# Kernel optimization log

Hardware: AMD Instinct MI355X
Metric: run time of the kernel (lower is better)

Reference implementation:

```python
import jax, jax.numpy as jnp
import numpy as np

EMBED_DIM = 768
FFN_DIM = 3072
N_WIRES = 10


def setup_inputs() -> dict:
    key = jax.random.key(0)
    ks = jax.random.split(key, 7)
    x = jax.random.normal(ks[0], (8, 2048, EMBED_DIM), dtype=jnp.float32)
    # map_to_wires: nn.Linear(embed_dim, n_wires, bias=False) -> weight [n_wires, embed_dim]
    W_map = jax.random.normal(ks[1], (N_WIRES, EMBED_DIM), dtype=jnp.float32) / np.sqrt(EMBED_DIM)
    # trainable RY rotation angles, one per wire
    theta = jax.random.uniform(ks[2], (N_WIRES,), dtype=jnp.float32, minval=-np.pi, maxval=np.pi)
    W1 = jax.random.normal(ks[3], (FFN_DIM, N_WIRES), dtype=jnp.float32) / np.sqrt(N_WIRES)
    b1 = jnp.zeros((FFN_DIM,), dtype=jnp.float32)
    W2 = jax.random.normal(ks[4], (EMBED_DIM, FFN_DIM), dtype=jnp.float32) / np.sqrt(FFN_DIM)
    b2 = jnp.zeros((EMBED_DIM,), dtype=jnp.float32)
    return {"x": x, "W_map": W_map, "theta": theta, "W1": W1, "b1": b1, "W2": W2, "b2": b2}


def reference(x, W_map, theta, W1, b1, W2, b2):
    batch, seq_len, embed_dim = x.shape
    x_flat = x.reshape(batch * seq_len, embed_dim)            # [F, E]
    x_wires = x_flat @ W_map.T                                 # [F, W]
    # Quantum circuit: per wire i, state RY(theta_i) RX(x_i) |0>.
    # All gates are single-qubit on the |0...0> product state, so the
    # register stays a product state and <Z_i> reduces exactly to
    # cos(theta_i) * cos(x_i) (same math as the full 2^n statevector sim).
    q_out = jnp.cos(theta)[None, :] * jnp.cos(x_wires)         # [F, W]
    h = jax.nn.relu(q_out @ W1.T + b1)                         # [F, FFN]
    out = h @ W2.T + b2                                        # [F, E]
    return out.reshape(batch, seq_len, embed_dim)
```

## Files before the change

### kernel.cpp

```cpp
#include <hip/hip_runtime.h>
#include <hip/hip_bf16.h>


typedef __attribute__((ext_vector_type(4))) float f32x4;
typedef __attribute__((ext_vector_type(8))) short bf16x8;

#define F_TOTAL 16384
#define E_DIM   768
#define FFN     3072

static __device__ __forceinline__ unsigned short f2bf(float f) {
    union { float f; unsigned int i; } v; v.f = f;
    unsigned int r = v.i + 0x7FFFu + ((v.i >> 16) & 1u);
    return (unsigned short)(r >> 16);
}
static __device__ __forceinline__ unsigned int pkbf(float a, float b) {
    __hip_bfloat162 h2 = __float22bfloat162_rn(float2{a, b});
    union { __hip_bfloat162 h; unsigned int u; } v; v.h = h2; return v.u;
}
static __device__ __forceinline__ void gload16(const void* g, void* l) {
    __builtin_amdgcn_global_load_lds((const __attribute__((address_space(1))) unsigned int*)g,
                                     (__attribute__((address_space(3))) unsigned int*)l,
                                     16, 0, 0);
}

__global__ __launch_bounds__(384) void kW2(const float* __restrict__ w2,
                                           unsigned short* __restrict__ w2b) {
    const int n = (int)blockIdx.x;
    const int c = (int)threadIdx.x;
    const float4* src = (const float4*)(w2 + (size_t)n * FFN + c * 8);
    float4 a = src[0], b = src[1];
    bf16x8 v;
    v[0] = (short)f2bf(a.x); v[1] = (short)f2bf(a.y);
    v[2] = (short)f2bf(a.z); v[3] = (short)f2bf(a.w);
    v[4] = (short)f2bf(b.x); v[5] = (short)f2bf(b.y);
    v[6] = (short)f2bf(b.z); v[7] = (short)f2bf(b.w);
    *(bf16x8*)(w2b + (size_t)n * FFN + (size_t)(c ^ (n & 7)) * 8) = v;
}

__global__ void kP(const float* __restrict__ w1,
                   const float* __restrict__ b1,
                   unsigned short* __restrict__ w1p) {
    int k = blockIdx.x * 256 + threadIdx.x;
    if (k >= FFN) return;
    float r[32];
#pragma unroll
    for (int w = 0; w < 10; ++w) r[w] = w1[k * 10 + w];
    r[10] = b1[k];
#pragma unroll
    for (int w = 11; w < 32; ++w) r[w] = 0.f;
#pragma unroll
    for (int c = 0; c < 4; ++c) {
        bf16x8 v;
#pragma unroll
        for (int e = 0; e < 8; ++e) v[e] = (short)f2bf(r[c * 8 + e]);
        *(bf16x8*)(w1p + (size_t)k * 32 + (size_t)((c ^ (k & 3)) * 8)) = v;
    }
}

__global__ __launch_bounds__(256) void kQ(const float* __restrict__ x,
                                          const float* __restrict__ wm,
                                          const float* __restrict__ th,
                                          unsigned short* __restrict__ qp) {
    __shared__ float wms[10 * 768];
    const int tid = (int)threadIdx.x;
    for (int i = tid; i < 10 * 768; i += 256) wms[i] = wm[i];
    __syncthreads();

    const int wv = tid >> 6, l = tid & 63;
    const int mbase = (int)blockIdx.x * 16 + wv * 4;
    const float thv = (l < 10) ? th[l] : 0.f;
    const float cth = __cosf(thv);

#pragma unroll
    for (int r = 0; r < 4; ++r) {
        const int m = mbase + r;
        const float4* xp = (const float4*)(x + (size_t)m * E_DIM);
        const float4 xa = xp[l], xb = xp[64 + l], xc = xp[128 + l];
        float s[10];
#pragma unroll
        for (int w = 0; w < 10; ++w) {
            const float4* wp = (const float4*)(wms + w * E_DIM);
            const float4 wa = wp[l], wb = wp[64 + l], wc = wp[128 + l];
            float t0 = xa.x * wa.x;
            float t1 = xa.y * wa.y;
            t0 = fmaf(xa.z, wa.z, t0); t1 = fmaf(xa.w, wa.w, t1);
            t0 = fmaf(xb.x, wb.x, t0); t1 = fmaf(xb.y, wb.y, t1);
            t0 = fmaf(xb.z, wb.z, t0); t1 = fmaf(xb.w, wb.w, t1);
            t0 = fmaf(xc.x, wc.x, t0); t1 = fmaf(xc.y, wc.y, t1);
            t0 = fmaf(xc.z, wc.z, t0); t1 = fmaf(xc.w, wc.w, t1);
            s[w] = t0 + t1;
        }
#pragma unroll
        for (int w = 0; w < 10; ++w) {
            float v = s[w];
            v += __shfl_xor(v, 1);  v += __shfl_xor(v, 2);  v += __shfl_xor(v, 4);
            v += __shfl_xor(v, 8);  v += __shfl_xor(v, 16); v += __shfl_xor(v, 32);
            s[w] = v;
        }
        if (l < 32) {
            float sv = 0.f;
#pragma unroll
            for (int w = 0; w < 10; ++w) sv = (l == w) ? s[w] : sv;
            float val = (l < 10) ? (cth * __cosf(sv)) : ((l == 10) ? 1.0f : 0.f);
            qp[(size_t)m * 32 + (size_t)((((l >> 3) ^ (m & 3)) * 8) + (l & 7))] = f2bf(val);
        }
    }
}

__global__ __launch_bounds__(512, 4) void kG(const unsigned short* __restrict__ w2b,
                                             const float* __restrict__ b2,
                                             const unsigned short* __restrict__ qp,
                                             const unsigned short* __restrict__ w1p,
                                             float* __restrict__ outp) {
    __shared__ __align__(16) unsigned short w2s[2][192 * 64];
    __shared__ __align__(16) unsigned short hs[128 * 64];

    const int tid = (int)threadIdx.x;
    const int wv = tid >> 6, l = tid & 63;
    const int bid = (int)blockIdx.x;
    const int x8 = bid & 7, yb = bid >> 3;
    const int m0 = ((x8 & 1) * 64 + yb) * 128;
    const int n0 = (x8 >> 1) * 192;

    const int rw = tid >> 3, cw = tid & 7;
    const int wr = wv >> 2, wc = wv & 3;

    int hwo[4];
    {
        const int hm = wv * 16 + (l & 15);
        const int kb = (l >> 4) * 4;
#pragma unroll
        for (int ki = 0; ki < 4; ++ki) {
            int k = ki * 16 + kb;
            int c = k >> 3;
            hwo[ki] = hm * 64 + ((c ^ (hm & 7)) * 8) + (k & 7);
        }
    }

#define STAGE(BUF, KT) do { int k0_ = (KT) * 64;                                   \
    _Pragma("unroll") for (int i_ = 0; i_ < 3; ++i_) {                             \
        int r_ = i_ * 64 + rw;                                                     \
        gload16(w2b + (size_t)(n0 + r_) * FFN + k0_ + (size_t)cw * 8,              \
                (unsigned short*)w2s[BUF] + i_ * 4096 + wv * 512); } } while (0)

#define LOADW1(D, KT, KI) do {                                                     \
    const unsigned short* a_ = w1p + (size_t)((KT) * 64 + (KI) * 16 + (l & 15)) * 32 \
                                   + (size_t)(((l >> 4) ^ (l & 3)) * 8);           \
    asm volatile("global_load_dwordx4 %0, %1, off" : "=v"(D) : "v"(a_)); } while (0)

    bf16x8 aq;
    {
        const unsigned short* qa = qp + (size_t)(m0 + wv * 16 + (l & 15)) * 32
                                      + (size_t)(((l >> 4) ^ (l & 3)) * 8);
        asm volatile("global_load_dwordx4 %0, %1, off" : "=v"(aq) : "v"(qa));
    }
    bf16x8 f0, f1, f2, f3, g0, g1, g2, g3;
    STAGE(0, 0);
    LOADW1(f0, 0, 0); LOADW1(f1, 0, 1); LOADW1(f2, 0, 2); LOADW1(f3, 0, 3);

    const f32x4 z4 = {0.f, 0.f, 0.f, 0.f};
    f32x4 acc[4][3];
#pragma unroll
    for (int a = 0; a < 4; ++a)
#pragma unroll
        for (int b = 0; b < 3; ++b) acc[a][b] = z4;

    int cur = 0;
    for (int t = 0; t < 48; ++t) {
        asm volatile("s_waitcnt vmcnt(0)" ::: "memory");
        __builtin_amdgcn_sched_barrier(0);
        __builtin_amdgcn_s_barrier();
        __builtin_amdgcn_sched_barrier(0);

        if (t < 47) {
            STAGE(cur ^ 1, t + 1);
            LOADW1(g0, t + 1, 0); LOADW1(g1, t + 1, 1);
            LOADW1(g2, t + 1, 2); LOADW1(g3, t + 1, 3);
        }

        {
            f32x4 hv0 = __builtin_amdgcn_mfma_f32_16x16x32_bf16(f0, aq, z4, 0, 0, 0);
            f32x4 hv1 = __builtin_amdgcn_mfma_f32_16x16x32_bf16(f1, aq, z4, 0, 0, 0);
            f32x4 hv2 = __builtin_amdgcn_mfma_f32_16x16x32_bf16(f2, aq, z4, 0, 0, 0);
            f32x4 hv3 = __builtin_amdgcn_mfma_f32_16x16x32_bf16(f3, aq, z4, 0, 0, 0);
            uint2 pw;
            pw.x = pkbf(fmaxf(hv0[0], 0.f), fmaxf(hv0[1], 0.f));
            pw.y = pkbf(fmaxf(hv0[2], 0.f), fmaxf(hv0[3], 0.f));
            *(uint2*)(hs + hwo[0]) = pw;
            pw.x = pkbf(fmaxf(hv1[0], 0.f), fmaxf(hv1[1], 0.f));
            pw.y = pkbf(fmaxf(hv1[2], 0.f), fmaxf(hv1[3], 0.f));
            *(uint2*)(hs + hwo[1]) = pw;
            pw.x = pkbf(fmaxf(hv2[0], 0.f), fmaxf(hv2[1], 0.f));
            pw.y = pkbf(fmaxf(hv2[2], 0.f), fmaxf(hv2[3], 0.f));
            *(uint2*)(hs + hwo[2]) = pw;
            pw.x = pkbf(fmaxf(hv3[0], 0.f), fmaxf(hv3[1], 0.f));
            pw.y = pkbf(fmaxf(hv3[2], 0.f), fmaxf(hv3[3], 0.f));
            *(uint2*)(hs + hwo[3]) = pw;
        }

        asm volatile("s_waitcnt lgkmcnt(0)" ::: "memory");
        __builtin_amdgcn_sched_barrier(0);
        __builtin_amdgcn_s_barrier();
        __builtin_amdgcn_sched_barrier(0);

        {
            const unsigned short* w2c = (const unsigned short*)w2s[cur];
#pragma unroll
            for (int kk2 = 0; kk2 < 2; ++kk2) {
                const int kc = kk2 * 4 + (l >> 4);
                bf16x8 af[4], bfr[3];
#pragma unroll
                for (int mi = 0; mi < 4; ++mi) {
                    int m_ = wr * 64 + mi * 16 + (l & 15);
                    af[mi] = *(const bf16x8*)(hs + m_ * 64 + ((kc ^ (m_ & 7)) * 8));
                }
#pragma unroll
                for (int ni = 0; ni < 3; ++ni) {
                    int n_ = wc * 48 + ni * 16 + (l & 15);
                    bfr[ni] = *(const bf16x8*)(w2c + n_ * 64 + ((kc ^ (n_ & 7)) * 8));
                }
                __builtin_amdgcn_s_setprio(1);
#pragma unroll
                for (int ni = 0; ni < 3; ++ni)
#pragma unroll
                    for (int mi = 0; mi < 4; ++mi)
                        acc[mi][ni] = __builtin_amdgcn_mfma_f32_16x16x32_bf16(af[mi], bfr[ni], acc[mi][ni], 0, 0, 0);
                __builtin_amdgcn_s_setprio(0);
            }
        }

        f0 = g0; f1 = g1; f2 = g2; f3 = g3;
        cur ^= 1;
    }
#undef STAGE
#undef LOADW1

#pragma unroll
    for (int ni = 0; ni < 3; ++ni) {
        int n = n0 + wc * 48 + ni * 16 + (l & 15);
        float b2v = b2[n];
#pragma unroll
        for (int mi = 0; mi < 4; ++mi) {
            int mb = m0 + wr * 64 + mi * 16 + (l >> 4) * 4;
#pragma unroll
            for (int jj = 0; jj < 4; ++jj)
                outp[(size_t)(mb + jj) * E_DIM + n] = acc[mi][ni][jj] + b2v;
        }
    }
}

extern "C" void kernel_launch(void* const* d_in, const int* in_sizes, int n_in,
                              void* d_out, int out_size, void* d_ws, size_t ws_size,
                              hipStream_t stream) {
    const float* x    = (const float*)d_in[0];
    const float* wmap = (const float*)d_in[1];
    const float* th   = (const float*)d_in[2];
    const float* w1   = (const float*)d_in[3];
    const float* b1   = (const float*)d_in[4];
    const float* w2   = (const float*)d_in[5];
    const float* b2   = (const float*)d_in[6];
    float* out = (float*)d_out;

    unsigned short* qp  = (unsigned short*)d_ws;
    unsigned short* w1p = qp + (size_t)F_TOTAL * 32;
    unsigned short* w2b = w1p + (size_t)FFN * 32;

    kW2<<<E_DIM, 384, 0, stream>>>(w2, w2b);
    kP<<<(FFN + 255) / 256, 256, 0, stream>>>(w1, b1, w1p);
    kQ<<<1024, 256, 0, stream>>>(x, wmap, th, qp);
    kG<<<512, 512, 0, stream>>>(w2b, b2, qp, w1p, out);
}
```

Before: 124.2 us.

## Load W2 fragments directly from global into registers instead of LDS staging

Drops the double-buffered LDS staging of W2 tiles via global_load_lds. Each wave now reads its W2 B-fragments straight from global memory into registers every iteration, and the W2 swizzle in the conversion kernel is removed to match. The W1 prefetch switches from inline asm to plain loads issued after the first GEMM. This frees LDS and a sync wait, but relies on L2/L1 to cover the W2 reads that the four row-waves repeat, and it loses explicit latency hiding since the loads are used in the same iteration.

```diff
diff --git a/kernel.cpp b/kernel.cpp
--- a/kernel.cpp
+++ b/kernel.cpp
@@ -17,11 +17,6 @@
 static __device__ __forceinline__ unsigned int pkbf(float a, float b) {
     __hip_bfloat162 h2 = __float22bfloat162_rn(float2{a, b});
     union { __hip_bfloat162 h; unsigned int u; } v; v.h = h2; return v.u;
-}
-static __device__ __forceinline__ void gload16(const void* g, void* l) {
-    __builtin_amdgcn_global_load_lds((const __attribute__((address_space(1))) unsigned int*)g,
-                                     (__attribute__((address_space(3))) unsigned int*)l,
-                                     16, 0, 0);
 }
 
 __global__ __launch_bounds__(384) void kW2(const float* __restrict__ w2,
@@ -35,7 +30,7 @@
     v[2] = (short)f2bf(a.z); v[3] = (short)f2bf(a.w);
     v[4] = (short)f2bf(b.x); v[5] = (short)f2bf(b.y);
     v[6] = (short)f2bf(b.z); v[7] = (short)f2bf(b.w);
-    *(bf16x8*)(w2b + (size_t)n * FFN + (size_t)(c ^ (n & 7)) * 8) = v;
+    *(bf16x8*)(w2b + (size_t)n * FFN + (size_t)c * 8) = v;
 }
 
 __global__ void kP(const float* __restrict__ w1,
@@ -113,7 +108,6 @@
                                              const unsigned short* __restrict__ qp,
                                              const unsigned short* __restrict__ w1p,
                                              float* __restrict__ outp) {
-    __shared__ __align__(16) unsigned short w2s[2][192 * 64];
     __shared__ __align__(16) unsigned short hs[128 * 64];
 
     const int tid = (int)threadIdx.x;
@@ -123,7 +117,6 @@
     const int m0 = ((x8 & 1) * 64 + yb) * 128;
     const int n0 = (x8 >> 1) * 192;
 
-    const int rw = tid >> 3, cw = tid & 7;
     const int wr = wv >> 2, wc = wv & 3;
 
     int hwo[4];
@@ -138,26 +131,18 @@
         }
     }
 
-#define STAGE(BUF, KT) do { int k0_ = (KT) * 64;                                   \
-    _Pragma("unroll") for (int i_ = 0; i_ < 3; ++i_) {                             \
-        int r_ = i_ * 64 + rw;                                                     \
-        gload16(w2b + (size_t)(n0 + r_) * FFN + k0_ + (size_t)cw * 8,              \
-                (unsigned short*)w2s[BUF] + i_ * 4096 + wv * 512); } } while (0)
-
-#define LOADW1(D, KT, KI) do {                                                     \
-    const unsigned short* a_ = w1p + (size_t)((KT) * 64 + (KI) * 16 + (l & 15)) * 32 \
-                                   + (size_t)(((l >> 4) ^ (l & 3)) * 8);           \
-    asm volatile("global_load_dwordx4 %0, %1, off" : "=v"(D) : "v"(a_)); } while (0)
-
-    bf16x8 aq;
-    {
-        const unsigned short* qa = qp + (size_t)(m0 + wv * 16 + (l & 15)) * 32
-                                      + (size_t)(((l >> 4) ^ (l & 3)) * 8);
-        asm volatile("global_load_dwordx4 %0, %1, off" : "=v"(aq) : "v"(qa));
-    }
-    bf16x8 f0, f1, f2, f3, g0, g1, g2, g3;
-    STAGE(0, 0);
-    LOADW1(f0, 0, 0); LOADW1(f1, 0, 1); LOADW1(f2, 0, 2); LOADW1(f3, 0, 3);
+    const unsigned short* p2[3];
+#pragma unroll
+    for (int ni = 0; ni < 3; ++ni)
+        p2[ni] = w2b + (size_t)(n0 + wc * 48 + ni * 16 + (l & 15)) * FFN + (l >> 4) * 8;
+    const unsigned short* p1 = w1p + (l & 15) * 32 + ((l >> 4) ^ (l & 3)) * 8;
+
+    bf16x8 aq = *(const bf16x8*)(qp + (size_t)(m0 + wv * 16 + (l & 15)) * 32
+                                    + (size_t)(((l >> 4) ^ (l & 3)) * 8));
+    bf16x8 f0 = *(const bf16x8*)(p1);
+    bf16x8 f1 = *(const bf16x8*)(p1 + 512);
+    bf16x8 f2 = *(const bf16x8*)(p1 + 1024);
+    bf16x8 f3 = *(const bf16x8*)(p1 + 1536);
 
     const f32x4 z4 = {0.f, 0.f, 0.f, 0.f};
     f32x4 acc[4][3];
@@ -166,18 +151,18 @@
 #pragma unroll
         for (int b = 0; b < 3; ++b) acc[a][b] = z4;
 
-    int cur = 0;
     for (int t = 0; t < 48; ++t) {
-        asm volatile("s_waitcnt vmcnt(0)" ::: "memory");
-        __builtin_amdgcn_sched_barrier(0);
+        asm volatile("" ::: "memory");
         __builtin_amdgcn_s_barrier();
         __builtin_amdgcn_sched_barrier(0);
 
-        if (t < 47) {
-            STAGE(cur ^ 1, t + 1);
-            LOADW1(g0, t + 1, 0); LOADW1(g1, t + 1, 1);
-            LOADW1(g2, t + 1, 2); LOADW1(g3, t + 1, 3);
-        }
+        const int k0e = t * 64;
+        bf16x8 b0  = *(const bf16x8*)(p2[0] + k0e);
+        bf16x8 b1_ = *(const bf16x8*)(p2[0] + k0e + 32);
+        bf16x8 b2_ = *(const bf16x8*)(p2[1] + k0e);
+        bf16x8 b3_ = *(const bf16x8*)(p2[1] + k0e + 32);
+        bf16x8 b4_ = *(const bf16x8*)(p2[2] + k0e);
+        bf16x8 b5_ = *(const bf16x8*)(p2[2] + k0e + 32);
 
         {
             f32x4 hv0 = __builtin_amdgcn_mfma_f32_16x16x32_bf16(f0, aq, z4, 0, 0, 0);
@@ -199,42 +184,48 @@
             *(uint2*)(hs + hwo[3]) = pw;
         }
 
+        {
+            const int tn = (t < 47) ? (t + 1) : 47;
+            const unsigned short* pn = p1 + (size_t)tn * 2048;
+            f0 = *(const bf16x8*)(pn);
+            f1 = *(const bf16x8*)(pn + 512);
+            f2 = *(const bf16x8*)(pn + 1024);
+            f3 = *(const bf16x8*)(pn + 1536);
+        }
+
         asm volatile("s_waitcnt lgkmcnt(0)" ::: "memory");
         __builtin_amdgcn_sched_barrier(0);
         __builtin_amdgcn_s_barrier();
         __builtin_amdgcn_sched_barrier(0);
 
-        {
-            const unsigned short* w2c = (const unsigned short*)w2s[cur];
-#pragma unroll
-            for (int kk2 = 0; kk2 < 2; ++kk2) {
-                const int kc = kk2 * 4 + (l >> 4);
-                bf16x8 af[4], bfr[3];
+#pragma unroll
+        for (int kk2 = 0; kk2 < 2; ++kk2) {
+            const int kc = kk2 * 4 + (l >> 4);
+            bf16x8 af[4];
+#pragma unroll
+            for (int mi = 0; mi < 4; ++mi) {
+                int m_ = wr * 64 + mi * 16 + (l & 15);
+                af[mi] = *(const bf16x8*)(hs + m_ * 64 + ((kc ^ (m_ & 7)) * 8));
+            }
+            __builtin_amdgcn_s_setprio(1);
+            if (kk2 == 0) {
 #pragma unroll
                 for (int mi = 0; mi < 4; ++mi) {
-                    int m_ = wr * 64 + mi * 16 + (l & 15);
-                    af[mi] = *(const bf16x8*)(hs + m_ * 64 + ((kc ^ (m_ & 7)) * 8));
+                    acc[mi][0] = __builtin_amdgcn_mfma_f32_16x16x32_bf16(af[mi], b0,  acc[mi][0], 0, 0, 0);
+                    acc[mi][1] = __builtin_amdgcn_mfma_f32_16x16x32_bf16(af[mi], b2_, acc[mi][1], 0, 0, 0);
+                    acc[mi][2] = __builtin_amdgcn_mfma_f32_16x16x32_bf16(af[mi], b4_, acc[mi][2], 0, 0, 0);
                 }
-#pragma unroll
-                for (int ni = 0; ni < 3; ++ni) {
-                    int n_ = wc * 48 + ni * 16 + (l & 15);
-                    bfr[ni] = *(const bf16x8*)(w2c + n_ * 64 + ((kc ^ (n_ & 7)) * 8));
+            } else {
+#pragma unroll
+                for (int mi = 0; mi < 4; ++mi) {
+                    acc[mi][0] = __builtin_amdgcn_mfma_f32_16x16x32_bf16(af[mi], b1_, acc[mi][0], 0, 0, 0);
+                    acc[mi][1] = __builtin_amdgcn_mfma_f32_16x16x32_bf16(af[mi], b3_, acc[mi][1], 0, 0, 0);
+                    acc[mi][2] = __builtin_amdgcn_mfma_f32_16x16x32_bf16(af[mi], b5_, acc[mi][2], 0, 0, 0);
                 }
-                __builtin_amdgcn_s_setprio(1);
-#pragma unroll
-                for (int ni = 0; ni < 3; ++ni)
-#pragma unroll
-                    for (int mi = 0; mi < 4; ++mi)
-                        acc[mi][ni] = __builtin_amdgcn_mfma_f32_16x16x32_bf16(af[mi], bfr[ni], acc[mi][ni], 0, 0, 0);
-                __builtin_amdgcn_s_setprio(0);
             }
-        }
-
-        f0 = g0; f1 = g1; f2 = g2; f3 = g3;
-        cur ^= 1;
-    }
-#undef STAGE
-#undef LOADW1
+            __builtin_amdgcn_s_setprio(0);
+        }
+    }
 
 #pragma unroll
     for (int ni = 0; ni < 3; ++ni) {
```

After: 192.4 us. 54.9% more time.
